# Performance work log

Hardware: AMD Instinct MI355X
Metric: run time of the kernel (lower is better)

Reference implementation:

```python
import jax, jax.numpy as jnp
import numpy as np

B, S, D = 8, 2048, 512

def setup_inputs() -> dict:
    key = jax.random.key(0)
    k1, k2 = jax.random.split(key)
    x = jax.random.normal(k1, (B, S, D), dtype=jnp.float32)
    # nn.Parameter(torch.rand(D, D)) -> uniform [0, 1)
    attn_matrix = jax.random.uniform(k2, (D, D), dtype=jnp.float32)
    return {"x": x, "attn_matrix": attn_matrix}

def reference(x, attn_matrix):
    # scalar = sqrt(last dim of x)
    scale = jnp.sqrt(jnp.asarray(x.shape[-1], dtype=x.dtype))
    # prod = x @ W @ x^T / sqrt(D)  -> [B, S, S]
    xw = jnp.einsum('bsd,de->bse', x, attn_matrix)
    prod = jnp.einsum('bse,bte->bst', xw, x) / scale
    scores = jax.nn.softmax(prod, axis=-1)
    out = jnp.einsum('bst,btd->bsd', scores, x)
    return out
```

## Files before the change

kernel.cpp:

```cpp
#include <hip/hip_runtime.h>
#include <math.h>

#define B_ 8
#define S_ 2048
#define D_ 512
#define HSZ (B_ * S_ * D_)

typedef _Float16 half8 __attribute__((ext_vector_type(8)));
typedef _Float16 half4h __attribute__((ext_vector_type(4)));
typedef __fp16 fp16x2 __attribute__((ext_vector_type(2)));
typedef float f32x4 __attribute__((ext_vector_type(4)));
typedef float f32x16 __attribute__((ext_vector_type(16)));
typedef unsigned int u32;

constexpr float INV_SCALE = 0.044194173824159216f;

__device__ __forceinline__ u32 pk16(float a, float b) {
    fp16x2 r = __builtin_amdgcn_cvt_pkrtz(a, b);
    union { fp16x2 h; u32 u; } U; U.h = r; return U.u;
}

__device__ __forceinline__ int offK(int t, int d) {
    return ((t >> 5) << 14) | (((d >> 7) & 3) << 12) | (((d >> 4) & 7) << 9) |
           ((t & 31) << 4) | (((d >> 3) & 1) << 3) | (d & 7);
}
__device__ __forceinline__ int offV(int t, int d) {
    return ((t >> 5) << 14) | (((d >> 7) & 3) << 12) | (((d >> 5) & 3) << 10) |
           (((t >> 4) & 1) << 9) | ((d & 31) << 4) | (((t >> 3) & 1) << 3) | (t & 7);
}
__device__ __forceinline__ int offWT(int n, int k) {
    return ((n >> 5) << 14) | ((k >> 4) << 9) | ((n & 31) << 4) |
           (((k >> 3) & 1) << 3) | (k & 7);
}

__global__ __launch_bounds__(256) void cvt_all(const float* __restrict__ x,
                                               const float* __restrict__ W,
                                               _Float16* __restrict__ xK,
                                               _Float16* __restrict__ xV,
                                               _Float16* __restrict__ WT) {
    __shared__ float T[64 * 65];
    const int tid = threadIdx.x;
    const int blk = blockIdx.x;

    const float* src;
    int t0, d0, isX, bofs = 0;
    if (blk < 2048) {
        int b = blk >> 8;
        int r = blk & 255;
        t0 = (r >> 3) * 64; d0 = (r & 7) * 64;
        src = x + (size_t)b * (S_ * D_);
        bofs = b * (S_ * D_);
        isX = 1;
    } else {
        int r = blk - 2048;
        t0 = (r >> 3) * 64; d0 = (r & 7) * 64;
        src = W;
        isX = 0;
    }

#pragma unroll
    for (int it = 0; it < 4; ++it) {
        int flat = it * 256 + tid;
        int row = flat >> 4, c4 = (flat & 15) * 4;
        float4 v = *(const float4*)(src + (size_t)(t0 + row) * 512 + d0 + c4);
        T[row * 65 + c4 + 0] = v.x; T[row * 65 + c4 + 1] = v.y;
        T[row * 65 + c4 + 2] = v.z; T[row * 65 + c4 + 3] = v.w;
        if (isX) {
            half4h h = { (_Float16)v.x, (_Float16)v.y, (_Float16)v.z, (_Float16)v.w };
            *(half4h*)(xK + bofs + offK(t0 + row, d0 + c4)) = h;
        }
    }
    __syncthreads();
#pragma unroll
    for (int it = 0; it < 2; ++it) {
        int flat = it * 256 + tid;
        int d = flat >> 3, c = (flat & 7) * 8;
        half8 hv;
#pragma unroll
        for (int j = 0; j < 8; ++j) hv[j] = (_Float16)T[(c + j) * 65 + d];
        if (isX)
            *(half8*)(xV + bofs + offV(t0 + c, d0 + d)) = hv;
        else
            *(half8*)(WT + offWT(d0 + d, t0 + c)) = hv;
    }
}

__global__ __launch_bounds__(256, 2) void gemm8(const _Float16* __restrict__ xK,
                                                const _Float16* __restrict__ WT,
                                                _Float16* __restrict__ qwh) {
    const int tid = threadIdx.x;
    const int w = tid >> 6, lane = tid & 63;
    const int r31 = lane & 31, hi = lane >> 5;
    const int laneoff = (r31 << 4) + (hi << 3);
    const int blk = blockIdx.x;
    const int nb = blk & 3;
    const int mb = blk >> 2;
    const int n0w = nb * 128 + w * 32;
    const int batch = mb >> 4;
    const int mt0 = (mb & 15) * 4;
    const size_t bb = (size_t)batch * (S_ * D_);

    half8 Bf[32];
    const _Float16* wb = WT + ((n0w >> 5) << 14) + laneoff;
#pragma unroll
    for (int kc = 0; kc < 32; ++kc) Bf[kc] = *(const half8*)(wb + (kc << 9));

    const _Float16* ab = xK + bb + laneoff;
    const int kk = n0w + r31;
    const int qterm = (((kk >> 7) & 3) << 12) + (((kk >> 4) & 7) << 9) +
                      (((kk >> 3) & 1) << 3) + (kk & 7);

#pragma unroll
    for (int mt = 0; mt < 4; ++mt) {
        const _Float16* at = ab + ((mt0 + mt) << 14);
        f32x16 ca, cb;
#pragma unroll
        for (int r = 0; r < 16; ++r) { ca[r] = 0.f; cb[r] = 0.f; }
#pragma unroll
        for (int kg = 0; kg < 4; ++kg) {
            half8 Af[8];
#pragma unroll
            for (int k8 = 0; k8 < 8; ++k8)
                Af[k8] = *(const half8*)(at + ((kg * 8 + k8) << 9));
#pragma unroll
            for (int k8 = 0; k8 < 8; k8 += 2) {
                ca = __builtin_amdgcn_mfma_f32_32x32x16_f16(Af[k8],     Bf[kg * 8 + k8],     ca, 0, 0, 0);
                cb = __builtin_amdgcn_mfma_f32_32x32x16_f16(Af[k8 + 1], Bf[kg * 8 + k8 + 1], cb, 0, 0, 0);
            }
        }
        _Float16* qp = qwh + bb + ((mt0 + mt) << 14) + qterm;
#pragma unroll
        for (int r = 0; r < 16; ++r) {
            int mrow = (r & 3) + ((r >> 2) << 3) + (hi << 2);
            qp[mrow << 4] = (_Float16)((ca[r] + cb[r]) * INV_SCALE);
        }
    }
}

__global__ __launch_bounds__(256, 2)
void flash8(const _Float16* __restrict__ xK, const _Float16* __restrict__ xV,
            const _Float16* __restrict__ qwh, float* __restrict__ out) {
    __shared__ __align__(16) unsigned char SMEM[69632];
    float* Sx = (float*)SMEM;

    const int tid = threadIdx.x;
    const int w = tid >> 6, lane = tid & 63;
    const int r31 = lane & 31, hi = lane >> 5;
    const int laneoff = (r31 << 4) + (hi << 3);
    const int d0w = w * 128;
    const int bx = blockIdx.x;
    const int b = bx & 7;
    const int q0 = (bx >> 3) * 32;
    const size_t xb = (size_t)b * (S_ * D_);

    half8 Qr[8];
    {
        const _Float16* qb = qwh + xb + ((q0 >> 5) << 14) + (w << 12) + laneoff;
#pragma unroll
        for (int kc = 0; kc < 8; ++kc)
            Qr[kc] = *(const half8*)(qb + (kc << 9));
    }

    const _Float16* kbase = xK + xb + (w << 12) + laneoff;
    const _Float16* vbase = xV + xb + (w << 12) + laneoff;

    half8 Ka[8], Kb2[8];
#pragma unroll
    for (int kc = 0; kc < 8; ++kc)
        Ka[kc] = *(const half8*)(kbase + (kc << 9));

    f32x16 O[4];
#pragma unroll
    for (int dc = 0; dc < 4; ++dc)
#pragma unroll
        for (int r = 0; r < 16; ++r) O[dc][r] = 0.f;
    float m = -1e30f, l = 0.f;

#define FBODY(TI, KC, KN) do {                                                  \
    const int tc_ = (TI);                                                       \
    const int tn_ = ((TI) + 1) & 63;                                            \
    const int p_ = (TI) & 1;                                                    \
                            \
    half8 Vc[8];                                                                \
    _Pragma("unroll") for (int dc = 0; dc < 4; ++dc)                            \
    _Pragma("unroll") for (int kh = 0; kh < 2; ++kh)                            \
        Vc[dc * 2 + kh] = *(const half8*)(vbase + (tc_ << 14) + (dc << 10) + (kh << 9)); \
                                  \
    f32x16 sa, sb;                                                              \
    _Pragma("unroll") for (int r = 0; r < 16; ++r) { sa[r] = 0.f; sb[r] = 0.f; }\
    _Pragma("unroll") for (int kc = 0; kc < 8; kc += 2) {                       \
        sa = __builtin_amdgcn_mfma_f32_32x32x16_f16(KC[kc],     Qr[kc],     sa, 0, 0, 0); \
        sb = __builtin_amdgcn_mfma_f32_32x32x16_f16(KC[kc + 1], Qr[kc + 1], sb, 0, 0, 0); \
    }                                                                           \
                             \
    _Pragma("unroll") for (int kc = 0; kc < 8; ++kc)                            \
        KN[kc] = *(const half8*)(kbase + (tn_ << 14) + (kc << 9));              \
    f32x16 sS = sa + sb;                                                        \
                 \
    {                                                                           \
        float* sxw = Sx + (p_ * 4 + w) * 1024;                                  \
        _Pragma("unroll") for (int r2 = 0; r2 < 4; ++r2) {                      \
            f32x4 v_ = { sS[4 * r2 + 0], sS[4 * r2 + 1], sS[4 * r2 + 2], sS[4 * r2 + 3] }; \
            *(f32x4*)&sxw[(r2 * 64 + lane) * 4] = v_;                           \
        }                                                                       \
    }                                                                           \
    __syncthreads();                    \
                                                                 \
    float sv[16];                                                               \
    _Pragma("unroll") for (int i = 0; i < 16; ++i) sv[i] = sS[i];               \
    _Pragma("unroll") for (int pw = 1; pw < 4; ++pw) {                          \
        const float* sxp = Sx + (p_ * 4 + (w ^ pw)) * 1024;                     \
        _Pragma("unroll") for (int r2 = 0; r2 < 4; ++r2) {                      \
            f32x4 pp = *(const f32x4*)&sxp[(r2 * 64 + lane) * 4];               \
            _Pragma("unroll") for (int j = 0; j < 4; ++j) sv[4 * r2 + j] += pp[j]; \
        }                                                                       \
    }                                                                           \
                               \
    float mt_ = sv[0];                                                          \
    _Pragma("unroll") for (int i = 1; i < 16; ++i) mt_ = fmaxf(mt_, sv[i]);     \
    mt_ = fmaxf(mt_, __shfl_xor(mt_, 32));                                      \
    if (__any(mt_ > m + 8.f)) {                                                 \
        float mn = fmaxf(m, mt_);                                               \
        float a_ = __expf(m - mn);                                              \
        l *= a_;                                                                \
        _Pragma("unroll") for (int dc = 0; dc < 4; ++dc)                        \
        _Pragma("unroll") for (int r = 0; r < 16; ++r) O[dc][r] *= a_;          \
        m = mn;                                                                 \
    }                                                                           \
    float pa[16]; float rs = 0.f;                                               \
    _Pragma("unroll") for (int i = 0; i < 16; ++i) { pa[i] = __expf(sv[i] - m); rs += pa[i]; } \
    l += rs + __shfl_xor(rs, 32);                                               \
              \
    u32 q16[8];                                                                 \
    _Pragma("unroll") for (int r2 = 0; r2 < 4; ++r2) {                          \
        q16[2 * r2 + 0] = pk16(pa[4 * r2 + 0], pa[4 * r2 + 1]);                 \
        q16[2 * r2 + 1] = pk16(pa[4 * r2 + 2], pa[4 * r2 + 3]);                 \
    }                                                                           \
    half8 Pf[2];                                                                \
    _Pragma("unroll") for (int kh = 0; kh < 2; ++kh) {                          \
        int r2o = 2 * kh + hi, r2s = 2 * kh + (hi ^ 1);                         \
        u32 rv0 = (u32)__shfl_xor((int)q16[2 * r2s + 0], 32);                   \
        u32 rv1 = (u32)__shfl_xor((int)q16[2 * r2s + 1], 32);                   \
        u32 o0 = q16[2 * r2o + 0], o1 = q16[2 * r2o + 1];                       \
        union { u32 u[4]; half8 v; } U_;                                        \
        U_.u[0] = hi ? rv0 : o0; U_.u[1] = hi ? rv1 : o1;                       \
        U_.u[2] = hi ? o0 : rv0; U_.u[3] = hi ? o1 : rv1;                       \
        Pf[kh] = U_.v;                                                          \
    }                                                                           \
                                                 \
    _Pragma("unroll") for (int dc = 0; dc < 4; ++dc) {                          \
        O[dc] = __builtin_amdgcn_mfma_f32_32x32x16_f16(Vc[dc * 2 + 0], Pf[0], O[dc], 0, 0, 0); \
        O[dc] = __builtin_amdgcn_mfma_f32_32x32x16_f16(Vc[dc * 2 + 1], Pf[1], O[dc], 0, 0, 0); \
    }                                                                           \
} while (0)

    for (int tp = 0; tp < 32; ++tp) {
        FBODY(2 * tp,     Ka,  Kb2);
        FBODY(2 * tp + 1, Kb2, Ka);
    }
#undef FBODY

    __syncthreads();

    {
        float inv = 1.0f / l;
        float* ew = (float*)SMEM + w * 4224;
#pragma unroll
        for (int dc = 0; dc < 4; ++dc)
#pragma unroll
            for (int r = 0; r < 16; ++r) {
                int dl = dc * 32 + (r & 3) + ((r >> 2) << 3) + (hi << 2);
                ew[r31 * 132 + dl] = O[dc][r] * inv;
            }
#pragma unroll
        for (int j = 0; j < 4; ++j) {
            int flat = j * 64 + lane;
            int qq = flat >> 3, c16 = (flat & 7) << 4;
            float* gp = out + xb + (size_t)(q0 + qq) * 512 + d0w + c16;
#pragma unroll
            for (int k = 0; k < 4; ++k)
                *(f32x4*)(gp + k * 4) = *(const f32x4*)&ew[qq * 132 + c16 + k * 4];
        }
    }
}

__global__ __launch_bounds__(256) void xw_gemm_f32(const float* __restrict__ A,
                                                   const float* __restrict__ W,
                                                   float* __restrict__ C) {
    __shared__ float As[16][65];
    __shared__ float Bs[16][64];
    const int tid = threadIdx.x;
    const int row0 = blockIdx.y * 64, col0 = blockIdx.x * 64;
    const int ty = tid / 16, tx = tid % 16;
    float acc[4][4] = {};
    const int ar = tid / 4, ak = (tid % 4) * 4, bk = tid / 16, bn = (tid % 16) * 4;
    for (int k0 = 0; k0 < 512; k0 += 16) {
        float4 a4 = *(const float4*)(A + (size_t)(row0 + ar) * 512 + k0 + ak);
        float4 b4 = *(const float4*)(W + (size_t)(k0 + bk) * 512 + col0 + bn);
        __syncthreads();
        As[ak + 0][ar] = a4.x; As[ak + 1][ar] = a4.y;
        As[ak + 2][ar] = a4.z; As[ak + 3][ar] = a4.w;
        *(float4*)&Bs[bk][bn] = b4;
        __syncthreads();
#pragma unroll
        for (int kk = 0; kk < 16; kk++) {
            float a[4], bv[4];
#pragma unroll
            for (int i = 0; i < 4; i++) a[i] = As[kk][ty * 4 + i];
#pragma unroll
            for (int j = 0; j < 4; j++) bv[j] = Bs[kk][tx * 4 + j];
#pragma unroll
            for (int i = 0; i < 4; i++)
#pragma unroll
                for (int j = 0; j < 4; j++) acc[i][j] += a[i] * bv[j];
        }
    }
#pragma unroll
    for (int i = 0; i < 4; i++) {
        float4 o = make_float4(acc[i][0] * INV_SCALE, acc[i][1] * INV_SCALE,
                               acc[i][2] * INV_SCALE, acc[i][3] * INV_SCALE);
        *(float4*)(C + (size_t)(row0 + ty * 4 + i) * 512 + col0 + tx * 4) = o;
    }
}

__global__ __launch_bounds__(256) void flash_f32(const float* __restrict__ x,
                                                 const float* __restrict__ qw,
                                                 float* __restrict__ out) {
    __shared__ float4 kt[16 * 136];
    const int tid = threadIdx.x;
    const int q = tid >> 3, g = tid & 7;
    const int blk = blockIdx.x;
    const int b = blk >> 6;
    const int qrow = (blk & 63) * 32 + q;
    const size_t xbase = (size_t)b * S_ * D_;
    float qwr[64];
    {
        const float4* p = (const float4*)(qw + xbase + (size_t)qrow * D_ + g * 64);
#pragma unroll
        for (int i4 = 0; i4 < 16; i4++) {
            float4 v = p[i4];
            qwr[4 * i4 + 0] = v.x; qwr[4 * i4 + 1] = v.y;
            qwr[4 * i4 + 2] = v.z; qwr[4 * i4 + 3] = v.w;
        }
    }
    float oa[64];
#pragma unroll
    for (int i = 0; i < 64; i++) oa[i] = 0.f;
    float m = -1e30f, l = 0.f;
    const float4* x4 = (const float4*)(x + xbase);
    for (int t0 = 0; t0 < S_; t0 += 16) {
        __syncthreads();
#pragma unroll
        for (int j = 0; j < 8; j++) {
            int f = tid + j * 256;
            int tt = f >> 7, c = f & 127;
            kt[tt * 136 + (c >> 4) * 17 + (c & 15)] = x4[(size_t)(t0 + tt) * 128 + c];
        }
        __syncthreads();
#pragma unroll 1
        for (int tt = 0; tt < 16; tt++) {
            float4 kv[16];
            const float4* kp = &kt[tt * 136 + g * 17];
#pragma unroll
            for (int i4 = 0; i4 < 16; i4++) kv[i4] = kp[i4];
            float s = 0.f;
#pragma unroll
            for (int i4 = 0; i4 < 16; i4++)
                s += qwr[4 * i4] * kv[i4].x + qwr[4 * i4 + 1] * kv[i4].y
                   + qwr[4 * i4 + 2] * kv[i4].z + qwr[4 * i4 + 3] * kv[i4].w;
            s += __shfl_xor(s, 1, 64); s += __shfl_xor(s, 2, 64); s += __shfl_xor(s, 4, 64);
            if (s > m) {
                float alpha = __expf(m - s);
                l *= alpha;
#pragma unroll
                for (int i = 0; i < 64; i++) oa[i] *= alpha;
                m = s;
            }
            float p = __expf(s - m);
            l += p;
#pragma unroll
            for (int i4 = 0; i4 < 16; i4++) {
                oa[4 * i4 + 0] += p * kv[i4].x; oa[4 * i4 + 1] += p * kv[i4].y;
                oa[4 * i4 + 2] += p * kv[i4].z; oa[4 * i4 + 3] += p * kv[i4].w;
            }
        }
    }
    float inv_l = 1.0f / l;
    float4* op = (float4*)(out + xbase + (size_t)qrow * D_ + g * 64);
#pragma unroll
    for (int i4 = 0; i4 < 16; i4++)
        op[i4] = make_float4(oa[4 * i4] * inv_l, oa[4 * i4 + 1] * inv_l,
                             oa[4 * i4 + 2] * inv_l, oa[4 * i4 + 3] * inv_l);
}

extern "C" void kernel_launch(void* const* d_in, const int* in_sizes, int n_in,
                              void* d_out, int out_size, void* d_ws, size_t ws_size,
                              hipStream_t stream) {
    const float* x = (const float*)d_in[0];
    const float* W = (const float*)d_in[1];
    float* out = (float*)d_out;

    const size_t F16 = (size_t)HSZ * sizeof(_Float16);
    const size_t off_qwh = 0;
    const size_t off_xK  = F16;
    const size_t off_xV  = 2 * F16;
    const size_t off_WT  = 3 * F16;
    const size_t base    = 3 * F16 + 512 * 512 * sizeof(_Float16);

    if (ws_size >= base) {
        _Float16* qwh = (_Float16*)((char*)d_ws + off_qwh);
        _Float16* xK  = (_Float16*)((char*)d_ws + off_xK);
        _Float16* xV  = (_Float16*)((char*)d_ws + off_xV);
        _Float16* WT  = (_Float16*)((char*)d_ws + off_WT);

        cvt_all<<<2112, 256, 0, stream>>>(x, W, xK, xV, WT);
        gemm8<<<512, 256, 0, stream>>>(xK, WT, qwh);
        flash8<<<512, 256, 0, stream>>>(xK, xV, qwh, out);
    } else {
        const size_t needf = (size_t)HSZ * sizeof(float);
        float* xw = (ws_size >= needf) ? (float*)d_ws : out;
        dim3 g1(512 / 64, (B_ * S_) / 64);
        xw_gemm_f32<<<g1, 256, 0, stream>>>(x, W, xw);
        flash_f32<<<B_ * (S_ / 32), 256, 0, stream>>>(x, xw, out);
    }
}
```

Before: 238.6 us.

## Double-buffer V tiles in registers and prioritise MFMA phases in flash kernel

The flash kernel now prefetches the next tile's V fragments into a second register set alongside K, instead of loading V for the current tile at the start of each iteration. The K and V loads for the next tile are issued after the barrier so they overlap the softmax and PV work. s_setprio brackets both MFMA blocks so waves doing matrix math get higher scheduling priority. This adds eight more half8 registers per lane, which under launch_bounds(256,2) could push register pressure or cause spills.

```diff
diff --git a/kernel.cpp b/kernel.cpp
--- a/kernel.cpp
+++ b/kernel.cpp
@@ -138,7 +138,7 @@
 }
 
 __global__ __launch_bounds__(256, 2)
-void flash8(const _Float16* __restrict__ xK, const _Float16* __restrict__ xV,
+void flash9(const _Float16* __restrict__ xK, const _Float16* __restrict__ xV,
             const _Float16* __restrict__ qwh, float* __restrict__ out) {
     __shared__ __align__(16) unsigned char SMEM[69632];
     float* Sx = (float*)SMEM;
@@ -164,10 +164,15 @@
     const _Float16* kbase = xK + xb + (w << 12) + laneoff;
     const _Float16* vbase = xV + xb + (w << 12) + laneoff;
 
-    half8 Ka[8], Kb2[8];
+    half8 Ka[8], Kb2[8], Va[8], Vb2[8];
 #pragma unroll
     for (int kc = 0; kc < 8; ++kc)
         Ka[kc] = *(const half8*)(kbase + (kc << 9));
+#pragma unroll
+    for (int dc = 0; dc < 4; ++dc)
+#pragma unroll
+        for (int kh = 0; kh < 2; ++kh)
+            Va[dc * 2 + kh] = *(const half8*)(vbase + (dc << 10) + (kh << 9));
 
     f32x16 O[4];
 #pragma unroll
@@ -176,25 +181,18 @@
         for (int r = 0; r < 16; ++r) O[dc][r] = 0.f;
     float m = -1e30f, l = 0.f;
 
-#define FBODY(TI, KC, KN) do {                                                  \
-    const int tc_ = (TI);                                                       \
+#define FBODY(TI, KC, KN, VC, VN) do {                                          \
     const int tn_ = ((TI) + 1) & 63;                                            \
     const int p_ = (TI) & 1;                                                    \
-                            \
-    half8 Vc[8];                                                                \
-    _Pragma("unroll") for (int dc = 0; dc < 4; ++dc)                            \
-    _Pragma("unroll") for (int kh = 0; kh < 2; ++kh)                            \
-        Vc[dc * 2 + kh] = *(const half8*)(vbase + (tc_ << 14) + (dc << 10) + (kh << 9)); \
                                   \
     f32x16 sa, sb;                                                              \
     _Pragma("unroll") for (int r = 0; r < 16; ++r) { sa[r] = 0.f; sb[r] = 0.f; }\
+    __builtin_amdgcn_s_setprio(1);                                              \
     _Pragma("unroll") for (int kc = 0; kc < 8; kc += 2) {                       \
         sa = __builtin_amdgcn_mfma_f32_32x32x16_f16(KC[kc],     Qr[kc],     sa, 0, 0, 0); \
         sb = __builtin_amdgcn_mfma_f32_32x32x16_f16(KC[kc + 1], Qr[kc + 1], sb, 0, 0, 0); \
     }                                                                           \
-                             \
-    _Pragma("unroll") for (int kc = 0; kc < 8; ++kc)                            \
-        KN[kc] = *(const half8*)(kbase + (tn_ << 14) + (kc << 9));              \
+    __builtin_amdgcn_s_setprio(0);                                              \
     f32x16 sS = sa + sb;                                                        \
                  \
     {                                                                           \
@@ -205,6 +203,12 @@
         }                                                                       \
     }                                                                           \
     __syncthreads();                    \
+                               \
+    _Pragma("unroll") for (int kc = 0; kc < 8; ++kc)                            \
+        KN[kc] = *(const half8*)(kbase + (tn_ << 14) + (kc << 9));              \
+    _Pragma("unroll") for (int dc = 0; dc < 4; ++dc)                            \
+    _Pragma("unroll") for (int kh = 0; kh < 2; ++kh)                            \
+        VN[dc * 2 + kh] = *(const half8*)(vbase + (tn_ << 14) + (dc << 10) + (kh << 9)); \
                                                                  \
     float sv[16];                                                               \
     _Pragma("unroll") for (int i = 0; i < 16; ++i) sv[i] = sS[i];               \
@@ -248,15 +252,17 @@
         Pf[kh] = U_.v;                                                          \
     }                                                                           \
                                                  \
+    __builtin_amdgcn_s_setprio(1);                                              \
     _Pragma("unroll") for (int dc = 0; dc < 4; ++dc) {                          \
-        O[dc] = __builtin_amdgcn_mfma_f32_32x32x16_f16(Vc[dc * 2 + 0], Pf[0], O[dc], 0, 0, 0); \
-        O[dc] = __builtin_amdgcn_mfma_f32_32x32x16_f16(Vc[dc * 2 + 1], Pf[1], O[dc], 0, 0, 0); \
-    }                                                                           \
+        O[dc] = __builtin_amdgcn_mfma_f32_32x32x16_f16(VC[dc * 2 + 0], Pf[0], O[dc], 0, 0, 0); \
+        O[dc] = __builtin_amdgcn_mfma_f32_32x32x16_f16(VC[dc * 2 + 1], Pf[1], O[dc], 0, 0, 0); \
+    }                                                                           \
+    __builtin_amdgcn_s_setprio(0);                                              \
 } while (0)
 
     for (int tp = 0; tp < 32; ++tp) {
-        FBODY(2 * tp,     Ka,  Kb2);
-        FBODY(2 * tp + 1, Kb2, Ka);
+        FBODY(2 * tp,     Ka,  Kb2, Va,  Vb2);
+        FBODY(2 * tp + 1, Kb2, Ka,  Vb2, Va);
     }
 #undef FBODY
 
@@ -415,7 +421,7 @@
 
         cvt_all<<<2112, 256, 0, stream>>>(x, W, xK, xV, WT);
         gemm8<<<512, 256, 0, stream>>>(xK, WT, qwh);
-        flash8<<<512, 256, 0, stream>>>(xK, xV, qwh, out);
+        flash9<<<512, 256, 0, stream>>>(xK, xV, qwh, out);
     } else {
         const size_t needf = (size_t)HSZ * sizeof(float);
         float* xw = (ws_size >= needf) ? (float*)d_ws : out;
```

After: 249.6 us. 1.05x slower.

## Split flash attention over key range into two partitions with combine kernel

Applied to the files above, without the earlier changes.

Splits the key/value sequence in two so the flash kernel launches 1024 blocks instead of 512. Each half writes an fp16 partial output plus the per-row running max and sum, and a new combine2 kernel merges the halves with log-sum-exp weights. Shared memory per block is halved by staging the epilogue in two phases, and launch bounds rise to 4 blocks per CU for higher occupancy. The cost is an extra kernel launch, extra global traffic for the fp16 partials, and fp16 rounding of the unnormalised partial outputs.

```diff
diff --git a/kernel.cpp b/kernel.cpp
--- a/kernel.cpp
+++ b/kernel.cpp
@@ -12,6 +12,7 @@
 typedef float f32x4 __attribute__((ext_vector_type(4)));
 typedef float f32x16 __attribute__((ext_vector_type(16)));
 typedef unsigned int u32;
+typedef u32 u32x4 __attribute__((ext_vector_type(4)));
 
 constexpr float INV_SCALE = 0.044194173824159216f;
 
@@ -137,10 +138,12 @@
     }
 }
 
-__global__ __launch_bounds__(256, 2)
-void flash8(const _Float16* __restrict__ xK, const _Float16* __restrict__ xV,
-            const _Float16* __restrict__ qwh, float* __restrict__ out) {
-    __shared__ __align__(16) unsigned char SMEM[69632];
+template <int SPLIT>
+__global__ __launch_bounds__(256, 4)
+void flashS(const _Float16* __restrict__ xK, const _Float16* __restrict__ xV,
+            const _Float16* __restrict__ qwh, float* __restrict__ out,
+            _Float16* __restrict__ Os, float* __restrict__ ml) {
+    __shared__ __align__(16) unsigned char SMEM[34816];
     float* Sx = (float*)SMEM;
 
     const int tid = threadIdx.x;
@@ -150,7 +153,10 @@
     const int d0w = w * 128;
     const int bx = blockIdx.x;
     const int b = bx & 7;
-    const int q0 = (bx >> 3) * 32;
+    const int q0 = ((bx >> 3) & 63) * 32;
+    const int s = (SPLIT == 2) ? (bx >> 9) : 0;
+    const int NT = 64 / SPLIT;
+    const int soff = s * NT;
     const size_t xb = (size_t)b * (S_ * D_);
 
     half8 Qr[8];
@@ -167,7 +173,7 @@
     half8 Ka[8], Kb2[8];
 #pragma unroll
     for (int kc = 0; kc < 8; ++kc)
-        Ka[kc] = *(const half8*)(kbase + (kc << 9));
+        Ka[kc] = *(const half8*)(kbase + (soff << 14) + (kc << 9));
 
     f32x16 O[4];
 #pragma unroll
@@ -177,10 +183,10 @@
     float m = -1e30f, l = 0.f;
 
 #define FBODY(TI, KC, KN) do {                                                  \
-    const int tc_ = (TI);                                                       \
-    const int tn_ = ((TI) + 1) & 63;                                            \
+    const int tc_ = soff + (TI);                                                \
+    const int tn_ = soff + (((TI) + 1) & (NT - 1));                             \
     const int p_ = (TI) & 1;                                                    \
-                            \
+               \
     half8 Vc[8];                                                                \
     _Pragma("unroll") for (int dc = 0; dc < 4; ++dc)                            \
     _Pragma("unroll") for (int kh = 0; kh < 2; ++kh)                            \
@@ -254,7 +260,7 @@
     }                                                                           \
 } while (0)
 
-    for (int tp = 0; tp < 32; ++tp) {
+    for (int tp = 0; tp < NT / 2; ++tp) {
         FBODY(2 * tp,     Ka,  Kb2);
         FBODY(2 * tp + 1, Kb2, Ka);
     }
@@ -264,23 +270,80 @@
 
     {
         float inv = 1.0f / l;
-        float* ew = (float*)SMEM + w * 4224;
-#pragma unroll
-        for (int dc = 0; dc < 4; ++dc)
-#pragma unroll
-            for (int r = 0; r < 16; ++r) {
-                int dl = dc * 32 + (r & 3) + ((r >> 2) << 3) + (hi << 2);
-                ew[r31 * 132 + dl] = O[dc][r] * inv;
+        float* ew = (float*)SMEM + w * 2176;
+        const int qq = lane >> 1, cs = (lane & 1) * 32;
+#pragma unroll
+        for (int ph = 0; ph < 2; ++ph) {
+#pragma unroll
+            for (int dc = 0; dc < 2; ++dc)
+#pragma unroll
+                for (int r = 0; r < 16; ++r) {
+                    int dl = dc * 32 + (r & 3) + ((r >> 2) << 3) + (hi << 2);
+                    ew[r31 * 68 + dl] = O[ph * 2 + dc][r] * inv;
+                }
+            if constexpr (SPLIT == 1) {
+                float* gp = out + xb + (size_t)(q0 + qq) * 512 + d0w + ph * 64 + cs;
+#pragma unroll
+                for (int k = 0; k < 8; ++k)
+                    *(f32x4*)(gp + 4 * k) = *(const f32x4*)&ew[qq * 68 + cs + 4 * k];
+            } else {
+                _Float16* op = Os + (size_t)s * HSZ +
+                               ((size_t)b * 2048 + q0 + qq) * 512 + d0w + ph * 64 + cs;
+#pragma unroll
+                for (int g = 0; g < 4; ++g) {
+                    f32x4 va = *(const f32x4*)&ew[qq * 68 + cs + 8 * g];
+                    f32x4 vb = *(const f32x4*)&ew[qq * 68 + cs + 8 * g + 4];
+                    u32x4 st = { pk16(va[0], va[1]), pk16(va[2], va[3]),
+                                 pk16(vb[0], vb[1]), pk16(vb[2], vb[3]) };
+                    *(u32x4*)(op + 8 * g) = st;
+                }
             }
-#pragma unroll
-        for (int j = 0; j < 4; ++j) {
-            int flat = j * 64 + lane;
-            int qq = flat >> 3, c16 = (flat & 7) << 4;
-            float* gp = out + xb + (size_t)(q0 + qq) * 512 + d0w + c16;
-#pragma unroll
-            for (int k = 0; k < 4; ++k)
-                *(f32x4*)(gp + k * 4) = *(const f32x4*)&ew[qq * 132 + c16 + k * 4];
-        }
+        }
+        if constexpr (SPLIT == 2) {
+            if (tid < 32) {
+                int idx = (((s << 3) + b) * 64 + (q0 >> 5)) * 64 + tid * 2;
+                ml[idx] = m; ml[idx + 1] = l;
+            }
+        }
+    }
+}
+
+__global__ __launch_bounds__(256) void combine2(const _Float16* __restrict__ Os,
+                                                const float* __restrict__ ml,
+                                                float* __restrict__ out) {
+    const int tid = threadIdx.x;
+    const int row = blockIdx.x * 8 + (tid >> 5);
+    const int t32 = tid & 31;
+    const int b = row >> 11, q = row & 2047;
+    const int mi = ((b * 64 + (q >> 5)) * 64) + (q & 31) * 2;
+    const float m0 = ml[mi], l0 = ml[mi + 1];
+    const float m1 = ml[(8 * 64 * 64) + mi], l1 = ml[(8 * 64 * 64) + mi + 1];
+    const float mm = fmaxf(m0, m1);
+    const float a0 = l0 * __expf(m0 - mm), a1 = l1 * __expf(m1 - mm);
+    const float inv = 1.0f / (a0 + a1);
+    const float w0 = a0 * inv, w1 = a1 * inv;
+
+    const size_t e = (size_t)row * 512 + t32 * 16;
+    half8 p0a = *(const half8*)(Os + e);
+    half8 p0b = *(const half8*)(Os + e + 8);
+    half8 p1a = *(const half8*)(Os + (size_t)HSZ + e);
+    half8 p1b = *(const half8*)(Os + (size_t)HSZ + e + 8);
+    float* gp = out + e;
+#pragma unroll
+    for (int g = 0; g < 2; ++g) {
+        f32x4 o;
+#pragma unroll
+        for (int j = 0; j < 4; ++j)
+            o[j] = w0 * (float)p0a[g * 4 + j] + w1 * (float)p1a[g * 4 + j];
+        *(f32x4*)(gp + g * 4) = o;
+    }
+#pragma unroll
+    for (int g = 0; g < 2; ++g) {
+        f32x4 o;
+#pragma unroll
+        for (int j = 0; j < 4; ++j)
+            o[j] = w0 * (float)p0b[g * 4 + j] + w1 * (float)p1b[g * 4 + j];
+        *(f32x4*)(gp + 8 + g * 4) = o;
     }
 }
 
@@ -406,6 +469,9 @@
     const size_t off_xV  = 2 * F16;
     const size_t off_WT  = 3 * F16;
     const size_t base    = 3 * F16 + 512 * 512 * sizeof(_Float16);
+    const size_t off_Os  = base;
+    const size_t off_ml  = base + 2 * F16;
+    const size_t need2   = base + 2 * F16 + (size_t)(2 * 8 * 64 * 64) * sizeof(float);
 
     if (ws_size >= base) {
         _Float16* qwh = (_Float16*)((char*)d_ws + off_qwh);
@@ -415,7 +481,14 @@
 
         cvt_all<<<2112, 256, 0, stream>>>(x, W, xK, xV, WT);
         gemm8<<<512, 256, 0, stream>>>(xK, WT, qwh);
-        flash8<<<512, 256, 0, stream>>>(xK, xV, qwh, out);
+        if (ws_size >= need2) {
+            _Float16* Os = (_Float16*)((char*)d_ws + off_Os);
+            float* ml    = (float*)((char*)d_ws + off_ml);
+            flashS<2><<<1024, 256, 0, stream>>>(xK, xV, qwh, out, Os, ml);
+            combine2<<<2048, 256, 0, stream>>>(Os, ml, out);
+        } else {
+            flashS<1><<<512, 256, 0, stream>>>(xK, xV, qwh, out, nullptr, nullptr);
+        }
     } else {
         const size_t needf = (size_t)HSZ * sizeof(float);
         float* xw = (ws_size >= needf) ? (float*)d_ws : out;
```

After: 848.7 us. 3.56x slower.

## Software-pipeline QK score computation one tile ahead in flash kernel

Applied to the files above, without the earlier changes.

Restructures the flash attention loop so the next tile's QK partial scores are computed and written to LDS while the current tile's softmax and PV accumulation run. A single barrier per iteration now serves both. The epilogue is split into two phases to halve the shared memory footprint. This adds register pressure from carrying the next scores and introduces a prologue and tail iteration.

```diff
diff --git a/kernel.cpp b/kernel.cpp
--- a/kernel.cpp
+++ b/kernel.cpp
@@ -12,6 +12,7 @@
 typedef float f32x4 __attribute__((ext_vector_type(4)));
 typedef float f32x16 __attribute__((ext_vector_type(16)));
 typedef unsigned int u32;
+typedef u32 u32x4 __attribute__((ext_vector_type(4)));
 
 constexpr float INV_SCALE = 0.044194173824159216f;
 
@@ -138,9 +139,9 @@
 }
 
 __global__ __launch_bounds__(256, 2)
-void flash8(const _Float16* __restrict__ xK, const _Float16* __restrict__ xV,
+void flashP(const _Float16* __restrict__ xK, const _Float16* __restrict__ xV,
             const _Float16* __restrict__ qwh, float* __restrict__ out) {
-    __shared__ __align__(16) unsigned char SMEM[69632];
+    __shared__ __align__(16) unsigned char SMEM[34816];
     float* Sx = (float*)SMEM;
 
     const int tid = threadIdx.x;
@@ -164,10 +165,33 @@
     const _Float16* kbase = xK + xb + (w << 12) + laneoff;
     const _Float16* vbase = xV + xb + (w << 12) + laneoff;
 
-    half8 Ka[8], Kb2[8];
+    half8 KA[8], KB[8];
+    f32x16 sS;
+
 #pragma unroll
     for (int kc = 0; kc < 8; ++kc)
-        Ka[kc] = *(const half8*)(kbase + (kc << 9));
+        KA[kc] = *(const half8*)(kbase + (kc << 9));
+    {
+        f32x16 s;
+#pragma unroll
+        for (int r = 0; r < 16; ++r) s[r] = 0.f;
+#pragma unroll
+        for (int kc = 0; kc < 8; ++kc)
+            s = __builtin_amdgcn_mfma_f32_32x32x16_f16(KA[kc], Qr[kc], s, 0, 0, 0);
+        sS = s;
+    }
+#pragma unroll
+    for (int kc = 0; kc < 8; ++kc)
+        KB[kc] = *(const half8*)(kbase + (1 << 14) + (kc << 9));
+    {
+        float* sxw = Sx + w * 1024;
+#pragma unroll
+        for (int r2 = 0; r2 < 4; ++r2) {
+            f32x4 v_ = { sS[4 * r2 + 0], sS[4 * r2 + 1], sS[4 * r2 + 2], sS[4 * r2 + 3] };
+            *(f32x4*)&sxw[(r2 * 64 + lane) * 4] = v_;
+        }
+    }
+    __syncthreads();
 
     f32x16 O[4];
 #pragma unroll
@@ -176,110 +200,121 @@
         for (int r = 0; r < 16; ++r) O[dc][r] = 0.f;
     float m = -1e30f, l = 0.f;
 
-#define FBODY(TI, KC, KN) do {                                                  \
-    const int tc_ = (TI);                                                       \
-    const int tn_ = ((TI) + 1) & 63;                                            \
-    const int p_ = (TI) & 1;                                                    \
-                            \
-    half8 Vc[8];                                                                \
-    _Pragma("unroll") for (int dc = 0; dc < 4; ++dc)                            \
-    _Pragma("unroll") for (int kh = 0; kh < 2; ++kh)                            \
-        Vc[dc * 2 + kh] = *(const half8*)(vbase + (tc_ << 14) + (dc << 10) + (kh << 9)); \
-                                  \
-    f32x16 sa, sb;                                                              \
-    _Pragma("unroll") for (int r = 0; r < 16; ++r) { sa[r] = 0.f; sb[r] = 0.f; }\
-    _Pragma("unroll") for (int kc = 0; kc < 8; kc += 2) {                       \
-        sa = __builtin_amdgcn_mfma_f32_32x32x16_f16(KC[kc],     Qr[kc],     sa, 0, 0, 0); \
-        sb = __builtin_amdgcn_mfma_f32_32x32x16_f16(KC[kc + 1], Qr[kc + 1], sb, 0, 0, 0); \
+#define SMX_HEAD(TI) \
+    half8 Vc[8]; \
+    _Pragma("unroll") for (int dc = 0; dc < 4; ++dc) \
+    _Pragma("unroll") for (int kh = 0; kh < 2; ++kh) \
+        Vc[dc * 2 + kh] = *(const half8*)(vbase + ((TI) << 14) + (dc << 10) + (kh << 9)); \
+    float sv[16]; \
+    { \
+        _Pragma("unroll") for (int i = 0; i < 16; ++i) sv[i] = sS[i]; \
+        _Pragma("unroll") for (int pw = 1; pw < 4; ++pw) { \
+            const float* sxp = Sx + (((TI) & 1) * 4 + (w ^ pw)) * 1024; \
+            _Pragma("unroll") for (int r2 = 0; r2 < 4; ++r2) { \
+                f32x4 pp = *(const f32x4*)&sxp[(r2 * 64 + lane) * 4]; \
+                _Pragma("unroll") for (int j = 0; j < 4; ++j) sv[4 * r2 + j] += pp[j]; \
+            } \
+        } \
+    } \
+    float mt_ = sv[0]; \
+    _Pragma("unroll") for (int i = 1; i < 16; ++i) mt_ = fmaxf(mt_, sv[i]); \
+    mt_ = fmaxf(mt_, __shfl_xor(mt_, 32)); \
+    if (__any(mt_ > m + 8.f)) { \
+        float mn = fmaxf(m, mt_); \
+        float a_ = __expf(m - mn); \
+        l *= a_; \
+        _Pragma("unroll") for (int dc = 0; dc < 4; ++dc) \
+        _Pragma("unroll") for (int r = 0; r < 16; ++r) O[dc][r] *= a_; \
+        m = mn; \
+    } \
+    float pa[16]; float rs = 0.f; \
+    _Pragma("unroll") for (int i = 0; i < 16; ++i) { pa[i] = __expf(sv[i] - m); rs += pa[i]; } \
+    l += rs + __shfl_xor(rs, 32);
+
+#define SMX_TAILPART \
+    u32 q16[8]; \
+    _Pragma("unroll") for (int r2 = 0; r2 < 4; ++r2) { \
+        q16[2 * r2 + 0] = pk16(pa[4 * r2 + 0], pa[4 * r2 + 1]); \
+        q16[2 * r2 + 1] = pk16(pa[4 * r2 + 2], pa[4 * r2 + 3]); \
+    } \
+    half8 Pf[2]; \
+    _Pragma("unroll") for (int kh = 0; kh < 2; ++kh) { \
+        int r2o = 2 * kh + hi, r2s = 2 * kh + (hi ^ 1); \
+        u32 rv0 = (u32)__shfl_xor((int)q16[2 * r2s + 0], 32); \
+        u32 rv1 = (u32)__shfl_xor((int)q16[2 * r2s + 1], 32); \
+        u32 o0 = q16[2 * r2o + 0], o1 = q16[2 * r2o + 1]; \
+        union { u32 u[4]; half8 v; } U_; \
+        U_.u[0] = hi ? rv0 : o0; U_.u[1] = hi ? rv1 : o1; \
+        U_.u[2] = hi ? o0 : rv0; U_.u[3] = hi ? o1 : rv1; \
+        Pf[kh] = U_.v; \
+    } \
+    _Pragma("unroll") for (int dc = 0; dc < 4; ++dc) { \
+        O[dc] = __builtin_amdgcn_mfma_f32_32x32x16_f16(Vc[dc * 2 + 0], Pf[0], O[dc], 0, 0, 0); \
+        O[dc] = __builtin_amdgcn_mfma_f32_32x32x16_f16(Vc[dc * 2 + 1], Pf[1], O[dc], 0, 0, 0); \
+    }
+
+#define PBODY(TI, KRD, KWR) do {                                                \
+    SMX_HEAD(TI)                                                                \
+                 \
+    f32x16 sn_;                                                                 \
+    {                                                                           \
+        f32x16 s_;                                                              \
+        _Pragma("unroll") for (int r = 0; r < 16; ++r) s_[r] = 0.f;             \
+        _Pragma("unroll") for (int kc = 0; kc < 8; ++kc)                        \
+            s_ = __builtin_amdgcn_mfma_f32_32x32x16_f16(KRD[kc], Qr[kc], s_, 0, 0, 0); \
+        sn_ = s_;                                                               \
     }                                                                           \
-                             \
-    _Pragma("unroll") for (int kc = 0; kc < 8; ++kc)                            \
-        KN[kc] = *(const half8*)(kbase + (tn_ << 14) + (kc << 9));              \
-    f32x16 sS = sa + sb;                                                        \
-                 \
+                                   \
     {                                                                           \
-        float* sxw = Sx + (p_ * 4 + w) * 1024;                                  \
+        const int tp2_ = ((TI) + 2) & 63;                                       \
+        _Pragma("unroll") for (int kc = 0; kc < 8; ++kc)                        \
+            KWR[kc] = *(const half8*)(kbase + (tp2_ << 14) + (kc << 9));        \
+    }                                                                           \
+    SMX_TAILPART                                                                \
+    sS = sn_;                                                                   \
+                                             \
+    {                                                                           \
+        float* sxw = Sx + ((((TI) + 1) & 1) * 4 + w) * 1024;                    \
         _Pragma("unroll") for (int r2 = 0; r2 < 4; ++r2) {                      \
             f32x4 v_ = { sS[4 * r2 + 0], sS[4 * r2 + 1], sS[4 * r2 + 2], sS[4 * r2 + 3] }; \
             *(f32x4*)&sxw[(r2 * 64 + lane) * 4] = v_;                           \
         }                                                                       \
     }                                                                           \
-    __syncthreads();                    \
-                                                                 \
-    float sv[16];                                                               \
-    _Pragma("unroll") for (int i = 0; i < 16; ++i) sv[i] = sS[i];               \
-    _Pragma("unroll") for (int pw = 1; pw < 4; ++pw) {                          \
-        const float* sxp = Sx + (p_ * 4 + (w ^ pw)) * 1024;                     \
-        _Pragma("unroll") for (int r2 = 0; r2 < 4; ++r2) {                      \
-            f32x4 pp = *(const f32x4*)&sxp[(r2 * 64 + lane) * 4];               \
-            _Pragma("unroll") for (int j = 0; j < 4; ++j) sv[4 * r2 + j] += pp[j]; \
-        }                                                                       \
-    }                                                                           \
-                               \
-    float mt_ = sv[0];                                                          \
-    _Pragma("unroll") for (int i = 1; i < 16; ++i) mt_ = fmaxf(mt_, sv[i]);     \
-    mt_ = fmaxf(mt_, __shfl_xor(mt_, 32));                                      \
-    if (__any(mt_ > m + 8.f)) {                                                 \
-        float mn = fmaxf(m, mt_);                                               \
-        float a_ = __expf(m - mn);                                              \
-        l *= a_;                                                                \
-        _Pragma("unroll") for (int dc = 0; dc < 4; ++dc)                        \
-        _Pragma("unroll") for (int r = 0; r < 16; ++r) O[dc][r] *= a_;          \
-        m = mn;                                                                 \
-    }                                                                           \
-    float pa[16]; float rs = 0.f;                                               \
-    _Pragma("unroll") for (int i = 0; i < 16; ++i) { pa[i] = __expf(sv[i] - m); rs += pa[i]; } \
-    l += rs + __shfl_xor(rs, 32);                                               \
-              \
-    u32 q16[8];                                                                 \
-    _Pragma("unroll") for (int r2 = 0; r2 < 4; ++r2) {                          \
-        q16[2 * r2 + 0] = pk16(pa[4 * r2 + 0], pa[4 * r2 + 1]);                 \
-        q16[2 * r2 + 1] = pk16(pa[4 * r2 + 2], pa[4 * r2 + 3]);                 \
-    }                                                                           \
-    half8 Pf[2];                                                                \
-    _Pragma("unroll") for (int kh = 0; kh < 2; ++kh) {                          \
-        int r2o = 2 * kh + hi, r2s = 2 * kh + (hi ^ 1);                         \
-        u32 rv0 = (u32)__shfl_xor((int)q16[2 * r2s + 0], 32);                   \
-        u32 rv1 = (u32)__shfl_xor((int)q16[2 * r2s + 1], 32);                   \
-        u32 o0 = q16[2 * r2o + 0], o1 = q16[2 * r2o + 1];                       \
-        union { u32 u[4]; half8 v; } U_;                                        \
-        U_.u[0] = hi ? rv0 : o0; U_.u[1] = hi ? rv1 : o1;                       \
-        U_.u[2] = hi ? o0 : rv0; U_.u[3] = hi ? o1 : rv1;                       \
-        Pf[kh] = U_.v;                                                          \
-    }                                                                           \
-                                                 \
-    _Pragma("unroll") for (int dc = 0; dc < 4; ++dc) {                          \
-        O[dc] = __builtin_amdgcn_mfma_f32_32x32x16_f16(Vc[dc * 2 + 0], Pf[0], O[dc], 0, 0, 0); \
-        O[dc] = __builtin_amdgcn_mfma_f32_32x32x16_f16(Vc[dc * 2 + 1], Pf[1], O[dc], 0, 0, 0); \
-    }                                                                           \
+    __syncthreads();                                                            \
 } while (0)
 
-    for (int tp = 0; tp < 32; ++tp) {
-        FBODY(2 * tp,     Ka,  Kb2);
-        FBODY(2 * tp + 1, Kb2, Ka);
-    }
-#undef FBODY
+    for (int tp = 0; tp < 31; ++tp) {
+        PBODY(2 * tp,     KB, KA);
+        PBODY(2 * tp + 1, KA, KB);
+    }
+    PBODY(62, KB, KA);
+    {
+        SMX_HEAD(63)
+        SMX_TAILPART
+    }
+#undef PBODY
+#undef SMX_HEAD
+#undef SMX_TAILPART
 
     __syncthreads();
 
     {
         float inv = 1.0f / l;
-        float* ew = (float*)SMEM + w * 4224;
-#pragma unroll
-        for (int dc = 0; dc < 4; ++dc)
-#pragma unroll
-            for (int r = 0; r < 16; ++r) {
-                int dl = dc * 32 + (r & 3) + ((r >> 2) << 3) + (hi << 2);
-                ew[r31 * 132 + dl] = O[dc][r] * inv;
-            }
-#pragma unroll
-        for (int j = 0; j < 4; ++j) {
-            int flat = j * 64 + lane;
-            int qq = flat >> 3, c16 = (flat & 7) << 4;
-            float* gp = out + xb + (size_t)(q0 + qq) * 512 + d0w + c16;
-#pragma unroll
-            for (int k = 0; k < 4; ++k)
-                *(f32x4*)(gp + k * 4) = *(const f32x4*)&ew[qq * 132 + c16 + k * 4];
+        float* ew = (float*)SMEM + w * 2176;
+        const int qq = lane >> 1, cs = (lane & 1) * 32;
+#pragma unroll
+        for (int ph = 0; ph < 2; ++ph) {
+#pragma unroll
+            for (int dc = 0; dc < 2; ++dc)
+#pragma unroll
+                for (int r = 0; r < 16; ++r) {
+                    int dl = dc * 32 + (r & 3) + ((r >> 2) << 3) + (hi << 2);
+                    ew[r31 * 68 + dl] = O[ph * 2 + dc][r] * inv;
+                }
+            float* gp = out + xb + (size_t)(q0 + qq) * 512 + d0w + ph * 64 + cs;
+#pragma unroll
+            for (int k = 0; k < 8; ++k)
+                *(f32x4*)(gp + 4 * k) = *(const f32x4*)&ew[qq * 68 + cs + 4 * k];
         }
     }
 }
@@ -415,7 +450,7 @@
 
         cvt_all<<<2112, 256, 0, stream>>>(x, W, xK, xV, WT);
         gemm8<<<512, 256, 0, stream>>>(xK, WT, qwh);
-        flash8<<<512, 256, 0, stream>>>(xK, xV, qwh, out);
+        flashP<<<512, 256, 0, stream>>>(xK, xV, qwh, out);
     } else {
         const size_t needf = (size_t)HSZ * sizeof(float);
         float* xw = (ws_size >= needf) ? (float*)d_ws : out;
```

New measurement: 231.3 us. 1.03x faster.
